# Performance work log

Hardware: AMD Instinct MI355X
Metric: run time of the kernel (lower is better)

The kernel has to match this reference:

```python
import jax, jax.numpy as jnp
import numpy as np

H, NH, HD, M, K = 768, 12, 64, 16, 4
BASE_LR, THETA = 1.0, 10000.0
EPS = 1e-5


def _freqs_cis():
    f = 1.0 / (THETA ** (np.arange(0, HD, 2)[: HD // 2].astype(np.float32) / HD))
    fr = np.outer(np.arange(2 * M), f).astype(np.float32)
    return jnp.asarray(np.complex64(np.cos(fr) + 1j * np.sin(fr)))  # [2M, HD//2]

FREQS = _freqs_cis()


def _rope(xq, xk, freqs):
    # xq, xk: [B,N,NH,HD]; freqs: [B,N,HD//2] complex64
    def rot(x):
        xr = x.astype(jnp.float32).reshape(*x.shape[:-1], -1, 2)
        xc = jax.lax.complex(xr[..., 0], xr[..., 1]) * freqs[:, :, None, :]
        return jnp.stack((jnp.real(xc), jnp.imag(xc)), -1).reshape(*x.shape)
    return rot(xq), rot(xk)


def _causal_conv(x, kern, bias):
    # x [B,N,C], kern [K,C]; module's left-pad + SAME conv => taps on x[t-K..t-1]
    B, N, C = x.shape
    y = jax.lax.conv_general_dilated(x, kern[:, None, :], (1,), [(K, 0)],
        dimension_numbers=('NWC', 'WIO', 'NWC'), feature_group_count=C)
    return y[:, :N] + bias


def _ln(x, g, b):
    mu = x.mean(-1, keepdims=True)
    v = x.var(-1, keepdims=True)
    return ((x - mu) / jnp.sqrt(v + EPS)) * g + b


def _ln_l2_bwd(x, tgt, g, b):
    # grad of 0.5*||LN(x) - tgt||^2 wrt x (fused, official TTT formulation)
    D = x.shape[-1]
    mu = x.mean(-1, keepdims=True)
    std = jnp.sqrt(x.var(-1, keepdims=True) + EPS)
    xh = (x - mu) / std
    gy = (g * xh + b - tgt) * g
    return (D * gy - gy.sum(-1, keepdims=True) - xh * (gy * xh).sum(-1, keepdims=True)) / (D * std)


def ttt_forward(hidden_states, position_ids, wq, wv, wo, wg,
                conv_q_kernel, conv_q_bias, conv_k_kernel, conv_k_bias,
                lr_w, lr_b, learnable_token_idx, ttt_gamma, ttt_beta,
                post_norm_scale, post_norm_bias, W1, b1):
    B, N, _ = hidden_states.shape
    nmb = N // M
    xqk = hidden_states @ wq  # shared pre-conv projection for Q and K
    XV = hidden_states @ wv
    XQ = _causal_conv(xqk, conv_q_kernel, conv_q_bias)
    XK = _causal_conv(xqk, conv_k_kernel, conv_k_bias)
    split = lambda x: x.reshape(B, N, NH, HD)
    XQ, XK, XV = split(XQ), split(XK), split(XV)
    freqs = FREQS[position_ids % M]  # [B,N,HD//2]
    XQ, XK = _rope(XQ, XK, freqs)
    # -> [nmb, B, NH, M, HD]
    mb = lambda x: x.reshape(B, nmb, M, NH, HD).transpose(1, 0, 3, 2, 4)
    XQ, XK, XV = mb(XQ), mb(XK), mb(XV)
    # eta [nmb,B,NH,M,M]: row i = token_idx lr schedule, col j = sigmoid lr of token j
    Xmb = hidden_states.reshape(B, nmb, M, H)
    lr = jax.nn.sigmoid(jnp.einsum('bnmw,hw->bhnm', Xmb, lr_w) + lr_b[None, :, None, None])
    tok = jnp.clip(learnable_token_idx + 1.0 / jnp.arange(1, M + 1, dtype=jnp.float32), 0.0)
    eta = (BASE_LR * tok)[None, None, None, :, None] * lr[:, :, :, None, :] / HD
    eta = eta.transpose(2, 0, 1, 3, 4)
    g = ttt_gamma[None]   # [1,NH,1,HD]
    bta = ttt_beta[None]
    tril = jnp.tril(jnp.ones((M, M), hidden_states.dtype))

    def step(carry, xs):
        W1c, b1c = carry  # [B,NH,HD,HD], [B,NH,1,HD]
        xq, xk, xv, et = xs
        Z1 = jnp.einsum('bhmd,bhde->bhme', xk, W1c) + b1c
        grad = _ln_l2_bwd(Z1, xv - xk, g, bta)  # [B,NH,M,HD]
        attn = tril * jnp.einsum('bhmd,bhnd->bhmn', xq, xk)
        b1_bar = b1c - jnp.einsum('bhmn,bhne->bhme', tril * et, grad)
        Z1_bar = jnp.einsum('bhmd,bhde->bhme', xq, W1c) - jnp.einsum('bhmn,bhne->bhme', et * attn, grad) + b1_bar
        last = et[..., -1, :, None]  # [B,NH,M,1] last row of eta
        W1n = W1c - jnp.einsum('bhmd,bhme->bhde', last * xk, grad)
        b1n = b1c - jnp.sum(last * grad, axis=-2, keepdims=True)
        return (W1n, b1n), xq + _ln(Z1_bar, g, bta)

    W1_0 = jnp.broadcast_to(W1[None], (B, NH, HD, HD))
    b1_0 = jnp.broadcast_to(b1[None], (B, NH, 1, HD))
    _, y = jax.lax.scan(step, (W1_0, b1_0), (XQ, XK, XV, eta))
    y = y.transpose(1, 0, 3, 2, 4).reshape(B, N, NH * HD)
    mu = y.mean(-1, keepdims=True)
    v = y.var(-1, keepdims=True)
    z = ((y - mu) / jnp.sqrt(v + EPS)) * post_norm_scale + post_norm_bias
    return (jax.nn.gelu(hidden_states @ wg) * z) @ wo


def setup_inputs() -> dict:
    key = jax.random.key(0)
    ks = jax.random.split(key, 10)
    B, N = 4, 2048
    s = 0.02
    return {
        'hidden_states': jax.random.normal(ks[0], (B, N, H), jnp.float32),
        'position_ids': jnp.arange(B * N, dtype=jnp.int32).reshape(B, N),
        'wq': jax.random.normal(ks[1], (H, NH * HD), jnp.float32) * s,
        'wv': jax.random.normal(ks[2], (H, NH * HD), jnp.float32) * s,
        'wo': jax.random.normal(ks[3], (NH * HD, H), jnp.float32) * s,
        'wg': jax.random.normal(ks[4], (H, H), jnp.float32) * s,
        'conv_q_kernel': jax.random.normal(ks[5], (K, H), jnp.float32) * s,
        'conv_q_bias': jnp.zeros((H,), jnp.float32),
        'conv_k_kernel': jax.random.normal(ks[6], (K, H), jnp.float32) * s,
        'conv_k_bias': jnp.zeros((H,), jnp.float32),
        'lr_w': jax.random.normal(ks[7], (NH, H), jnp.float32) * s,
        'lr_b': jnp.zeros((NH,), jnp.float32),
        'learnable_token_idx': jnp.zeros((M,), jnp.float32),
        'ttt_gamma': jnp.ones((NH, 1, HD), jnp.float32),
        'ttt_beta': jnp.zeros((NH, 1, HD), jnp.float32),
        'post_norm_scale': jnp.ones((NH * HD,), jnp.float32),
        'post_norm_bias': jnp.zeros((NH * HD,), jnp.float32),
        'W1': jax.random.normal(ks[8], (NH, HD, HD), jnp.float32) * s,
        'b1': jnp.zeros((NH, 1, HD), jnp.float32),
    }


def reference(hidden_states, position_ids, wq, wv, wo, wg,
              conv_q_kernel, conv_q_bias, conv_k_kernel, conv_k_bias,
              lr_w, lr_b, learnable_token_idx, ttt_gamma, ttt_beta,
              post_norm_scale, post_norm_bias, W1, b1):
    return ttt_forward(hidden_states, position_ids, wq, wv, wo, wg,
                       conv_q_kernel, conv_q_bias, conv_k_kernel, conv_k_bias,
                       lr_w, lr_b, learnable_token_idx, ttt_gamma, ttt_beta,
                       post_norm_scale, post_norm_bias, W1, b1)
```

## Files before the change

### kernel.cpp

```cpp
#include <hip/hip_runtime.h>
#include <math.h>

#define Hdim 768
#define NH 12
#define HD 64
#define MM 16
#define KK 4
#define Bb 4
#define Nn 2048
#define NMB 128
#define EPSV 1e-5f
#define PLD 2320
#define NCOLS 2316

__device__ float g_tab[1024];
__device__ float g_Wcat[(size_t)Hdim * PLD + 512];
__device__ float g_P[(size_t)Bb * Nn * PLD + 512];
__device__ float g_XQ[(size_t)Bb * NH * Nn * HD];
__device__ float g_XK[(size_t)Bb * NH * Nn * HD];
__device__ float g_XV[(size_t)Bb * NH * Nn * HD];
__device__ float g_lrv[(size_t)Bb * NH * Nn];
__device__ float g_y[(size_t)Bb * Nn * Hdim];

template <int CTRL>
__device__ __forceinline__ float dpp_mov(float x) {
    return __int_as_float(__builtin_amdgcn_update_dpp(
        0, __float_as_int(x), CTRL, 0xF, 0xF, true));
}
__device__ __forceinline__ float red16_dpp(float x) {
    x += dpp_mov<0xB1>(x);
    x += dpp_mov<0x4E>(x);
    x += dpp_mov<0x141>(x);
    x += dpp_mov<0x140>(x);
    return x;
}

__global__ __launch_bounds__(256) void prep_kernel(
    const float* __restrict__ wq, const float* __restrict__ wv,
    const float* __restrict__ wg, const float* __restrict__ lrw,
    float* __restrict__ Wcat, float* __restrict__ tab)
{
    int idx0 = blockIdx.x * 256 + threadIdx.x;
    if (idx0 < 512) {
        int pos = idx0 >> 5, k = idx0 & 31;
        double f = pow(10000.0, -(double)k / 32.0);
        double a = (double)pos * f;
        tab[2 * idx0 + 0] = (float)cos(a);
        tab[2 * idx0 + 1] = (float)sin(a);
    }
    const int total = Hdim * PLD;
    for (int i = idx0; i < total; i += 2048 * 256) {
        int k = i / PLD, j = i - k * PLD;
        float v;
        if (j < 768)       v = wq[k * 768 + j];
        else if (j < 1536) v = wv[k * 768 + (j - 768)];
        else if (j < 2304) v = wg[k * 768 + (j - 1536)];
        else if (j < NCOLS) v = lrw[(j - 2304) * 768 + k];
        else v = 0.f;
        Wcat[i] = v;
    }
}

__global__ __launch_bounds__(256) void gemm_tiled(
    const float* __restrict__ A, int lda,
    const float* __restrict__ Bm, int ldb,
    float* __restrict__ C, int ldc,
    int M, int N, int K)
{
    __shared__ float As[16][132];
    __shared__ float Bs[16][132];
    const int tid = threadIdx.x;
    const int tx = tid & 15, ty = tid >> 4;
    const int row0 = blockIdx.y * 128;
    const int col0 = blockIdx.x * 128;
    const int r_lo = ty * 4, c_lo = tx * 4;

    float acc[8][8];
#pragma unroll
    for (int i = 0; i < 8; ++i)
#pragma unroll
        for (int j = 0; j < 8; ++j) acc[i][j] = 0.f;

    for (int kt = 0; kt < K; kt += 16) {
#pragma unroll
        for (int i = 0; i < 2; ++i) {
            int id = tid + i * 256;
            int r = id >> 2, kq = (id & 3) * 4;
            const float4 a = *reinterpret_cast<const float4*>(
                &A[(size_t)(row0 + r) * lda + kt + kq]);
            As[kq + 0][r] = a.x; As[kq + 1][r] = a.y;
            As[kq + 2][r] = a.z; As[kq + 3][r] = a.w;
        }
#pragma unroll
        for (int i = 0; i < 2; ++i) {
            int id = tid + i * 256;
            int kr = id >> 5, jq = (id & 31) * 4;
            const float4 bv = *reinterpret_cast<const float4*>(
                &Bm[(size_t)(kt + kr) * ldb + col0 + jq]);
            *reinterpret_cast<float4*>(&Bs[kr][jq]) = bv;
        }
        __syncthreads();
#pragma unroll
        for (int k = 0; k < 16; ++k) {
            float a[8], bb[8];
            *reinterpret_cast<float4*>(&a[0]) = *reinterpret_cast<float4*>(&As[k][r_lo]);
            *reinterpret_cast<float4*>(&a[4]) = *reinterpret_cast<float4*>(&As[k][64 + r_lo]);
            *reinterpret_cast<float4*>(&bb[0]) = *reinterpret_cast<float4*>(&Bs[k][c_lo]);
            *reinterpret_cast<float4*>(&bb[4]) = *reinterpret_cast<float4*>(&Bs[k][64 + c_lo]);
#pragma unroll
            for (int i = 0; i < 8; ++i)
#pragma unroll
                for (int j = 0; j < 8; ++j)
                    acc[i][j] = fmaf(a[i], bb[j], acc[i][j]);
        }
        __syncthreads();
    }
#pragma unroll
    for (int i = 0; i < 8; ++i) {
        int rr = row0 + ((i < 4) ? (r_lo + i) : (64 + r_lo + i - 4));
        if (rr >= M) continue;
#pragma unroll
        for (int jb = 0; jb < 2; ++jb) {
            int cc = col0 + jb * 64 + c_lo;
            if (cc + 3 < N) {
                *reinterpret_cast<float4*>(&C[(size_t)rr * ldc + cc]) =
                    make_float4(acc[i][jb * 4 + 0], acc[i][jb * 4 + 1],
                                acc[i][jb * 4 + 2], acc[i][jb * 4 + 3]);
            } else {
#pragma unroll
                for (int jj = 0; jj < 4; ++jj)
                    if (cc + jj < N) C[(size_t)rr * ldc + cc + jj] = acc[i][jb * 4 + jj];
            }
        }
    }
}

__global__ __launch_bounds__(256) void conv_rope_kernel(
    const float* __restrict__ P, const int* __restrict__ pid,
    const float* __restrict__ cqk, const float* __restrict__ cqb,
    const float* __restrict__ ckk, const float* __restrict__ ckb,
    const float* __restrict__ lr_b, const float* __restrict__ tab,
    float* __restrict__ XQp, float* __restrict__ XKp, float* __restrict__ XVp,
    float* __restrict__ lrv)
{
    const int t = blockIdx.x;
    const int b = t >> 11, n = t & 2047;
    const int tid = threadIdx.x;
    __shared__ float xq_s[768], xk_s[768];
    const size_t rowP = (size_t)t * PLD;

#pragma unroll
    for (int i = 0; i < 3; ++i) {
        int c = tid + i * 256;
        float aq = cqb[c], ak = ckb[c];
#pragma unroll
        for (int w = 0; w < 4; ++w) {
            int np = n + w - 4;
            if (np >= 0) {
                float x = P[(size_t)(t + w - 4) * PLD + c];
                aq = fmaf(cqk[w * 768 + c], x, aq);
                ak = fmaf(ckk[w * 768 + c], x, ak);
            }
        }
        xq_s[c] = aq; xk_s[c] = ak;
        int h = c >> 6, d = c & 63;
        XVp[((size_t)(b * NH + h)) * (Nn * HD) + n * 64 + d] = P[rowP + 768 + c];
    }
    if (tid < NH) {
        float x = P[rowP + 2304 + tid] + lr_b[tid];
        lrv[((size_t)(b * NH + tid)) * Nn + n] = 1.f / (1.f + expf(-x));
    }
    __syncthreads();
    const int pos = pid[t] & 15;
    for (int p = tid; p < 384; p += 256) {
        int h = p >> 5, k = p & 31;
        float cv = tab[(pos * 32 + k) * 2 + 0];
        float sv = tab[(pos * 32 + k) * 2 + 1];
        int c0 = h * 64 + 2 * k;
        size_t base = ((size_t)(b * NH + h)) * (Nn * HD) + n * 64 + 2 * k;
        float x0 = xq_s[c0], x1 = xq_s[c0 + 1];
        XQp[base + 0] = x0 * cv - x1 * sv;
        XQp[base + 1] = x0 * sv + x1 * cv;
        x0 = xk_s[c0]; x1 = xk_s[c0 + 1];
        XKp[base + 0] = x0 * cv - x1 * sv;
        XKp[base + 1] = x0 * sv + x1 * cv;
    }
}

__global__ __launch_bounds__(256) void ttt_scan_kernel(
    const float* __restrict__ XQp, const float* __restrict__ XKp,
    const float* __restrict__ XVp, const float* __restrict__ lrv,
    const float* __restrict__ W1g, const float* __restrict__ b1g,
    const float* __restrict__ gam, const float* __restrict__ bet,
    const float* __restrict__ tokidx, float* __restrict__ ybuf)
{
    const int h = blockIdx.x, b = blockIdx.y;
    const int bh = b * NH + h;
    const int tid = threadIdx.x;
    const int e = tid & 63, q = tid >> 6;
    const int q16 = q * 16;

    __shared__ float xq_s[2][16][68], xk_s[2][16][68], xv_s[2][16][68];
    __shared__ float grad_s[16][68];
    __shared__ float part[2][4][16][64];
    __shared__ float b1_s[2][64], g_s[64], bt_s[64];
    __shared__ float lrs_s[2][16], tokv_s[16], alpha_s[16];
    __shared__ float coef_s[16][17];

    float W1own[16];
#pragma unroll
    for (int r = 0; r < 16; ++r)
        W1own[r] = W1g[h * 4096 + (q16 + r) * 64 + e];
    if (tid < 64) {
        b1_s[0][tid] = b1g[h * 64 + tid];
        g_s[tid]  = gam[h * 64 + tid];
        bt_s[tid] = bet[h * 64 + tid];
    }
    if (tid < 16)
        tokv_s[tid] = fmaxf(tokidx[tid] + 1.f / (float)(tid + 1), 0.f);

    const size_t base = (size_t)bh * (Nn * HD);
    const int m_st = tid >> 4, d_st = (tid & 15) * 4;

    float4 pfq, pfk, pfv;
    float pflr = 0.f;
    {
        size_t off = base + (size_t)tid * 4;
        pfq = *reinterpret_cast<const float4*>(XQp + off);
        pfk = *reinterpret_cast<const float4*>(XKp + off);
        pfv = *reinterpret_cast<const float4*>(XVp + off);
        if (tid < 16) pflr = lrv[(size_t)bh * Nn + tid];
    }
    *reinterpret_cast<float4*>(&xq_s[0][m_st][d_st]) = pfq;
    *reinterpret_cast<float4*>(&xk_s[0][m_st][d_st]) = pfk;
    *reinterpret_cast<float4*>(&xv_s[0][m_st][d_st]) = pfv;
    if (tid < 16) lrs_s[0][tid] = pflr;
    __syncthreads();

    float zb[4];
    int cur = 0;

    for (int c = 0; c < NMB; ++c) {
        const int nxt = cur ^ 1;

        {
            const int cn = (c < NMB - 1) ? (c + 1) : c;
            size_t off = base + (size_t)cn * 1024 + tid * 4;
            pfq = *reinterpret_cast<const float4*>(XQp + off);
            pfk = *reinterpret_cast<const float4*>(XKp + off);
            pfv = *reinterpret_cast<const float4*>(XVp + off);
            if (tid < 16) pflr = lrv[(size_t)bh * Nn + cn * 16 + tid];
        }
#pragma unroll
        for (int m = 0; m < 16; ++m) {
            float xkv[16], xqv[16];
            *reinterpret_cast<float4*>(&xkv[0])  = *reinterpret_cast<float4*>(&xk_s[cur][m][q16 + 0]);
            *reinterpret_cast<float4*>(&xkv[4])  = *reinterpret_cast<float4*>(&xk_s[cur][m][q16 + 4]);
            *reinterpret_cast<float4*>(&xkv[8])  = *reinterpret_cast<float4*>(&xk_s[cur][m][q16 + 8]);
            *reinterpret_cast<float4*>(&xkv[12]) = *reinterpret_cast<float4*>(&xk_s[cur][m][q16 + 12]);
            *reinterpret_cast<float4*>(&xqv[0])  = *reinterpret_cast<float4*>(&xq_s[cur][m][q16 + 0]);
            *reinterpret_cast<float4*>(&xqv[4])  = *reinterpret_cast<float4*>(&xq_s[cur][m][q16 + 4]);
            *reinterpret_cast<float4*>(&xqv[8])  = *reinterpret_cast<float4*>(&xq_s[cur][m][q16 + 8]);
            *reinterpret_cast<float4*>(&xqv[12]) = *reinterpret_cast<float4*>(&xq_s[cur][m][q16 + 12]);
            float az = 0.f, aq = 0.f;
#pragma unroll
            for (int r = 0; r < 16; ++r) {
                az = fmaf(xkv[r], W1own[r], az);
                aq = fmaf(xqv[r], W1own[r], aq);
            }
            part[0][q][m][e] = az;
            part[1][q][m][e] = aq;
        }
        __syncthreads();

        {
            *reinterpret_cast<float4*>(&xq_s[nxt][m_st][d_st]) = pfq;
            *reinterpret_cast<float4*>(&xk_s[nxt][m_st][d_st]) = pfk;
            *reinterpret_cast<float4*>(&xv_s[nxt][m_st][d_st]) = pfv;
            if (tid < 16) lrs_s[nxt][tid] = pflr;

            const int m = tid >> 4, e0 = (tid & 15) * 4;
            float4 p0 = *reinterpret_cast<float4*>(&part[0][0][m][e0]);
            float4 p1 = *reinterpret_cast<float4*>(&part[0][1][m][e0]);
            float4 p2 = *reinterpret_cast<float4*>(&part[0][2][m][e0]);
            float4 p3 = *reinterpret_cast<float4*>(&part[0][3][m][e0]);
            float4 q0 = *reinterpret_cast<float4*>(&part[1][0][m][e0]);
            float4 q1 = *reinterpret_cast<float4*>(&part[1][1][m][e0]);
            float4 q2 = *reinterpret_cast<float4*>(&part[1][2][m][e0]);
            float4 q3 = *reinterpret_cast<float4*>(&part[1][3][m][e0]);
            float z1[4];
            z1[0] = b1_s[cur][e0 + 0] + p0.x + p1.x + p2.x + p3.x;
            z1[1] = b1_s[cur][e0 + 1] + p0.y + p1.y + p2.y + p3.y;
            z1[2] = b1_s[cur][e0 + 2] + p0.z + p1.z + p2.z + p3.z;
            z1[3] = b1_s[cur][e0 + 3] + p0.w + p1.w + p2.w + p3.w;
            zb[0] = q0.x + q1.x + q2.x + q3.x;
            zb[1] = q0.y + q1.y + q2.y + q3.y;
            zb[2] = q0.z + q1.z + q2.z + q3.z;
            zb[3] = q0.w + q1.w + q2.w + q3.w;

            float lsum = red16_dpp(z1[0] + z1[1] + z1[2] + z1[3]);
            const float mu = lsum * (1.f / 64.f);
            float lss = 0.f;
#pragma unroll
            for (int jj = 0; jj < 4; ++jj) { float d = z1[jj] - mu; lss += d * d; }
            lss = red16_dpp(lss);
            const float rstd = 1.f / sqrtf(lss * (1.f / 64.f) + EPSV);
            float gy[4], xh[4], sgy = 0.f, sgx = 0.f;
#pragma unroll
            for (int jj = 0; jj < 4; ++jj) {
                int ee = e0 + jj;
                xh[jj] = (z1[jj] - mu) * rstd;
                float tgt = xv_s[cur][m][ee] - xk_s[cur][m][ee];
                gy[jj] = (g_s[ee] * xh[jj] + bt_s[ee] - tgt) * g_s[ee];
                sgy += gy[jj]; sgx += gy[jj] * xh[jj];
            }
            sgy = red16_dpp(sgy); sgx = red16_dpp(sgx);
            const float sc = rstd * (1.f / 64.f);
#pragma unroll
            for (int jj = 0; jj < 4; ++jj)
                grad_s[m][e0 + jj] = (64.f * gy[jj] - sgy - xh[jj] * sgx) * sc;

            const int i3 = m, j3 = (tid & 15);
            float cf = 0.f;
            if (j3 <= i3) {
                float s = 0.f;
#pragma unroll
                for (int d = 0; d < 64; d += 4) {
                    float4 a  = *reinterpret_cast<float4*>(&xq_s[cur][i3][d]);
                    float4 bq = *reinterpret_cast<float4*>(&xk_s[cur][j3][d]);
                    s += a.x * bq.x + a.y * bq.y + a.z * bq.z + a.w * bq.w;
                }
                cf = tokv_s[i3] * lrs_s[cur][j3] * (1.f / 64.f) * (1.f + s);
            }
            coef_s[i3][j3] = cf;
            if (tid < 16) alpha_s[tid] = tokv_s[15] * lrs_s[cur][tid] * (1.f / 64.f);
        }
        __syncthreads();

        {
            const int m = tid >> 4, e0 = (tid & 15) * 4;
            float zf[4];
#pragma unroll
            for (int jj = 0; jj < 4; ++jj) zf[jj] = zb[jj] + b1_s[cur][e0 + jj];
            for (int j = 0; j <= m; ++j) {
                float cfv = coef_s[m][j];
                float4 g4 = *reinterpret_cast<float4*>(&grad_s[j][e0]);
                zf[0] = fmaf(-cfv, g4.x, zf[0]);
                zf[1] = fmaf(-cfv, g4.y, zf[1]);
                zf[2] = fmaf(-cfv, g4.z, zf[2]);
                zf[3] = fmaf(-cfv, g4.w, zf[3]);
            }
            float lsum = red16_dpp(zf[0] + zf[1] + zf[2] + zf[3]);
            const float mu = lsum * (1.f / 64.f);
            float lss = 0.f;
#pragma unroll
            for (int jj = 0; jj < 4; ++jj) { float d = zf[jj] - mu; lss += d * d; }
            lss = red16_dpp(lss);
            const float rstd = 1.f / sqrtf(lss * (1.f / 64.f) + EPSV);
            float ov[4];
#pragma unroll
            for (int jj = 0; jj < 4; ++jj) {
                int ee = e0 + jj;
                ov[jj] = xq_s[cur][m][ee] + ((zf[jj] - mu) * rstd * g_s[ee] + bt_s[ee]);
            }
            size_t yoff = (size_t)(b * Nn + c * 16 + m) * 768 + h * 64 + e0;
            *reinterpret_cast<float4*>(&ybuf[yoff]) =
                make_float4(ov[0], ov[1], ov[2], ov[3]);
        }
        {
#pragma unroll
            for (int m = 0; m < 16; ++m) {
                float f = alpha_s[m] * grad_s[m][e];
                float xkv[16];
                *reinterpret_cast<float4*>(&xkv[0])  = *reinterpret_cast<float4*>(&xk_s[cur][m][q16 + 0]);
                *reinterpret_cast<float4*>(&xkv[4])  = *reinterpret_cast<float4*>(&xk_s[cur][m][q16 + 4]);
                *reinterpret_cast<float4*>(&xkv[8])  = *reinterpret_cast<float4*>(&xk_s[cur][m][q16 + 8]);
                *reinterpret_cast<float4*>(&xkv[12]) = *reinterpret_cast<float4*>(&xk_s[cur][m][q16 + 12]);
#pragma unroll
                for (int r = 0; r < 16; ++r)
                    W1own[r] = fmaf(-f, xkv[r], W1own[r]);
            }
            if (q == 0) {
                float sb = 0.f;
#pragma unroll
                for (int m = 0; m < 16; ++m)
                    sb += alpha_s[m] * grad_s[m][e];
                b1_s[nxt][e] = b1_s[cur][e] - sb;
            }
        }
        __syncthreads();
        cur = nxt;
    }
}

__global__ __launch_bounds__(256) void post_gate_kernel(
    const float* __restrict__ ybuf, const float* __restrict__ P,
    const float* __restrict__ ps, const float* __restrict__ pb,
    float* __restrict__ u)
{
    const int t = blockIdx.x;
    const int tid = threadIdx.x;
    __shared__ float red_a[4], red_b[4];
    float v[3];
    float lsum = 0.f;
#pragma unroll
    for (int i = 0; i < 3; ++i) {
        int c = tid + i * 256;
        v[i] = ybuf[(size_t)t * 768 + c];
        lsum += v[i];
    }
#pragma unroll
    for (int m = 1; m < 64; m <<= 1) lsum += __shfl_xor(lsum, m);
    if ((tid & 63) == 0) red_a[tid >> 6] = lsum;
    __syncthreads();
    const float mu = (red_a[0] + red_a[1] + red_a[2] + red_a[3]) * (1.f / 768.f);
    float lv = 0.f;
#pragma unroll
    for (int i = 0; i < 3; ++i) { float d = v[i] - mu; lv += d * d; }
#pragma unroll
    for (int m = 1; m < 64; m <<= 1) lv += __shfl_xor(lv, m);
    if ((tid & 63) == 0) red_b[tid >> 6] = lv;
    __syncthreads();
    const float var = (red_b[0] + red_b[1] + red_b[2] + red_b[3]) * (1.f / 768.f);
    const float rstd = 1.f / sqrtf(var + EPSV);
#pragma unroll
    for (int i = 0; i < 3; ++i) {
        int c = tid + i * 256;
        float g = P[(size_t)t * PLD + 1536 + c];
        float gl = 0.5f * g * (1.f + tanhf(0.7978845608028654f * (g + 0.044715f * g * g * g)));
        u[(size_t)t * 768 + c] = gl * ((v[i] - mu) * rstd * ps[c] + pb[c]);
    }
}

extern "C" void kernel_launch(void* const* d_in, const int* in_sizes, int n_in,
                              void* d_out, int out_size, void* d_ws, size_t ws_size,
                              hipStream_t stream)
{
    const float* hs   = (const float*)d_in[0];
    const int*   pid  = (const int*)  d_in[1];
    const float* wq   = (const float*)d_in[2];
    const float* wv   = (const float*)d_in[3];
    const float* wo   = (const float*)d_in[4];
    const float* wg   = (const float*)d_in[5];
    const float* cqk  = (const float*)d_in[6];
    const float* cqb  = (const float*)d_in[7];
    const float* ckk  = (const float*)d_in[8];
    const float* ckb  = (const float*)d_in[9];
    const float* lrw  = (const float*)d_in[10];
    const float* lrb  = (const float*)d_in[11];
    const float* lti  = (const float*)d_in[12];
    const float* gam  = (const float*)d_in[13];
    const float* bet  = (const float*)d_in[14];
    const float* ps   = (const float*)d_in[15];
    const float* pb   = (const float*)d_in[16];
    const float* W1g  = (const float*)d_in[17];
    const float* b1g  = (const float*)d_in[18];
    float* out = (float*)d_out;
    (void)d_ws; (void)ws_size; (void)in_sizes; (void)n_in; (void)out_size;

    float *tab = nullptr, *Wcat = nullptr, *P = nullptr, *XQp = nullptr,
          *XKp = nullptr, *XVp = nullptr, *lrv = nullptr, *ybuf = nullptr;
    hipGetSymbolAddress((void**)&tab,  HIP_SYMBOL(g_tab));
    hipGetSymbolAddress((void**)&Wcat, HIP_SYMBOL(g_Wcat));
    hipGetSymbolAddress((void**)&P,    HIP_SYMBOL(g_P));
    hipGetSymbolAddress((void**)&XQp,  HIP_SYMBOL(g_XQ));
    hipGetSymbolAddress((void**)&XKp,  HIP_SYMBOL(g_XK));
    hipGetSymbolAddress((void**)&XVp,  HIP_SYMBOL(g_XV));
    hipGetSymbolAddress((void**)&lrv,  HIP_SYMBOL(g_lrv));
    hipGetSymbolAddress((void**)&ybuf, HIP_SYMBOL(g_y));
    float* ubuf = XQp;

    hipLaunchKernelGGL(prep_kernel, dim3(2048), dim3(256), 0, stream,
                       wq, wv, wg, lrw, Wcat, tab);
    hipLaunchKernelGGL(gemm_tiled, dim3(19, 64), dim3(256), 0, stream,
                       hs, Hdim, Wcat, PLD, P, PLD, Bb * Nn, NCOLS, Hdim);
    hipLaunchKernelGGL(conv_rope_kernel, dim3(Bb * Nn), dim3(256), 0, stream,
                       P, pid, cqk, cqb, ckk, ckb, lrb, tab, XQp, XKp, XVp, lrv);
    hipLaunchKernelGGL(ttt_scan_kernel, dim3(NH, Bb), dim3(256), 0, stream,
                       XQp, XKp, XVp, lrv, W1g, b1g, gam, bet, lti, ybuf);
    hipLaunchKernelGGL(post_gate_kernel, dim3(Bb * Nn), dim3(256), 0, stream,
                       ybuf, P, ps, pb, ubuf);
    hipLaunchKernelGGL(gemm_tiled, dim3(6, 64), dim3(256), 0, stream,
                       ubuf, Hdim, wo, Hdim, out, Hdim, Bb * Nn, Hdim, Hdim);
}
```

Baseline: 1.262 ms.

## Read scan inputs straight from global memory instead of LDS double-buffering

Drops the shared-memory double buffers for XQ/XK/XV/lr in the TTT scan kernel and reads chunk rows directly from global memory. The row offset is forced wave-uniform with readfirstlane, so these reads can become scalar loads, and the part buffer is padded to 68 columns. This is meant to cut LDS traffic, shared-memory footprint and the store/prefetch staging, but it removes the explicit prefetch of the next chunk. It also reloads the same data several times per chunk from global or cache, which risks exposed memory latency on the serial scan.

```diff
diff --git a/kernel.cpp b/kernel.cpp
--- a/kernel.cpp
+++ b/kernel.cpp
@@ -199,12 +199,12 @@
     const int tid = threadIdx.x;
     const int e = tid & 63, q = tid >> 6;
     const int q16 = q * 16;
-
-    __shared__ float xq_s[2][16][68], xk_s[2][16][68], xv_s[2][16][68];
+    const int q16u = __builtin_amdgcn_readfirstlane(q16);
+
+    __shared__ float part[2][4][16][68];
     __shared__ float grad_s[16][68];
-    __shared__ float part[2][4][16][64];
     __shared__ float b1_s[2][64], g_s[64], bt_s[64];
-    __shared__ float lrs_s[2][16], tokv_s[16], alpha_s[16];
+    __shared__ float tokv_s[16], alpha_s[16];
     __shared__ float coef_s[16][17];
 
     float W1own[16];
@@ -220,65 +220,61 @@
         tokv_s[tid] = fmaxf(tokidx[tid] + 1.f / (float)(tid + 1), 0.f);
 
     const size_t base = (size_t)bh * (Nn * HD);
-    const int m_st = tid >> 4, d_st = (tid & 15) * 4;
-
-    float4 pfq, pfk, pfv;
-    float pflr = 0.f;
-    {
-        size_t off = base + (size_t)tid * 4;
-        pfq = *reinterpret_cast<const float4*>(XQp + off);
-        pfk = *reinterpret_cast<const float4*>(XKp + off);
-        pfv = *reinterpret_cast<const float4*>(XVp + off);
-        if (tid < 16) pflr = lrv[(size_t)bh * Nn + tid];
-    }
-    *reinterpret_cast<float4*>(&xq_s[0][m_st][d_st]) = pfq;
-    *reinterpret_cast<float4*>(&xk_s[0][m_st][d_st]) = pfk;
-    *reinterpret_cast<float4*>(&xv_s[0][m_st][d_st]) = pfv;
-    if (tid < 16) lrs_s[0][tid] = pflr;
+    const float* __restrict__ lrC0 = lrv + (size_t)bh * Nn;
     __syncthreads();
 
     float zb[4];
-    int cur = 0;
 
     for (int c = 0; c < NMB; ++c) {
-        const int nxt = cur ^ 1;
+        const int cur = c & 1, nxt = cur ^ 1;
+        const float* __restrict__ xkC = XKp + base + (size_t)c * 1024;
+        const float* __restrict__ xqC = XQp + base + (size_t)c * 1024;
+        const float* __restrict__ xvC = XVp + base + (size_t)c * 1024;
+        const float* __restrict__ lrC = lrC0 + c * 16;
+
+#pragma unroll
+        for (int mb = 0; mb < 4; ++mb) {
+            float xrow[4][16];
+#pragma unroll
+            for (int mm = 0; mm < 4; ++mm) {
+                const float* rp = xkC + (mb * 4 + mm) * 64 + q16u;
+                *reinterpret_cast<float4*>(&xrow[mm][0])  = *reinterpret_cast<const float4*>(rp + 0);
+                *reinterpret_cast<float4*>(&xrow[mm][4])  = *reinterpret_cast<const float4*>(rp + 4);
+                *reinterpret_cast<float4*>(&xrow[mm][8])  = *reinterpret_cast<const float4*>(rp + 8);
+                *reinterpret_cast<float4*>(&xrow[mm][12]) = *reinterpret_cast<const float4*>(rp + 12);
+            }
+#pragma unroll
+            for (int mm = 0; mm < 4; ++mm) {
+                float az = 0.f;
+#pragma unroll
+                for (int r = 0; r < 16; ++r)
+                    az = fmaf(xrow[mm][r], W1own[r], az);
+                part[0][q][mb * 4 + mm][e] = az;
+            }
+        }
+#pragma unroll
+        for (int mb = 0; mb < 4; ++mb) {
+            float xrow[4][16];
+#pragma unroll
+            for (int mm = 0; mm < 4; ++mm) {
+                const float* rp = xqC + (mb * 4 + mm) * 64 + q16u;
+                *reinterpret_cast<float4*>(&xrow[mm][0])  = *reinterpret_cast<const float4*>(rp + 0);
+                *reinterpret_cast<float4*>(&xrow[mm][4])  = *reinterpret_cast<const float4*>(rp + 4);
+                *reinterpret_cast<float4*>(&xrow[mm][8])  = *reinterpret_cast<const float4*>(rp + 8);
+                *reinterpret_cast<float4*>(&xrow[mm][12]) = *reinterpret_cast<const float4*>(rp + 12);
+            }
+#pragma unroll
+            for (int mm = 0; mm < 4; ++mm) {
+                float aq = 0.f;
+#pragma unroll
+                for (int r = 0; r < 16; ++r)
+                    aq = fmaf(xrow[mm][r], W1own[r], aq);
+                part[1][q][mb * 4 + mm][e] = aq;
+            }
+        }
+        __syncthreads();
 
         {
-            const int cn = (c < NMB - 1) ? (c + 1) : c;
-            size_t off = base + (size_t)cn * 1024 + tid * 4;
-            pfq = *reinterpret_cast<const float4*>(XQp + off);
-            pfk = *reinterpret_cast<const float4*>(XKp + off);
-            pfv = *reinterpret_cast<const float4*>(XVp + off);
-            if (tid < 16) pflr = lrv[(size_t)bh * Nn + cn * 16 + tid];
-        }
-#pragma unroll
-        for (int m = 0; m < 16; ++m) {
-            float xkv[16], xqv[16];
-            *reinterpret_cast<float4*>(&xkv[0])  = *reinterpret_cast<float4*>(&xk_s[cur][m][q16 + 0]);
-            *reinterpret_cast<float4*>(&xkv[4])  = *reinterpret_cast<float4*>(&xk_s[cur][m][q16 + 4]);
-            *reinterpret_cast<float4*>(&xkv[8])  = *reinterpret_cast<float4*>(&xk_s[cur][m][q16 + 8]);
-            *reinterpret_cast<float4*>(&xkv[12]) = *reinterpret_cast<float4*>(&xk_s[cur][m][q16 + 12]);
-            *reinterpret_cast<float4*>(&xqv[0])  = *reinterpret_cast<float4*>(&xq_s[cur][m][q16 + 0]);
-            *reinterpret_cast<float4*>(&xqv[4])  = *reinterpret_cast<float4*>(&xq_s[cur][m][q16 + 4]);
-            *reinterpret_cast<float4*>(&xqv[8])  = *reinterpret_cast<float4*>(&xq_s[cur][m][q16 + 8]);
-            *reinterpret_cast<float4*>(&xqv[12]) = *reinterpret_cast<float4*>(&xq_s[cur][m][q16 + 12]);
-            float az = 0.f, aq = 0.f;
-#pragma unroll
-            for (int r = 0; r < 16; ++r) {
-                az = fmaf(xkv[r], W1own[r], az);
-                aq = fmaf(xqv[r], W1own[r], aq);
-            }
-            part[0][q][m][e] = az;
-            part[1][q][m][e] = aq;
-        }
-        __syncthreads();
-
-        {
-            *reinterpret_cast<float4*>(&xq_s[nxt][m_st][d_st]) = pfq;
-            *reinterpret_cast<float4*>(&xk_s[nxt][m_st][d_st]) = pfk;
-            *reinterpret_cast<float4*>(&xv_s[nxt][m_st][d_st]) = pfv;
-            if (tid < 16) lrs_s[nxt][tid] = pflr;
-
             const int m = tid >> 4, e0 = (tid & 15) * 4;
             float4 p0 = *reinterpret_cast<float4*>(&part[0][0][m][e0]);
             float4 p1 = *reinterpret_cast<float4*>(&part[0][1][m][e0]);
@@ -305,13 +301,17 @@
             for (int jj = 0; jj < 4; ++jj) { float d = z1[jj] - mu; lss += d * d; }
             lss = red16_dpp(lss);
             const float rstd = 1.f / sqrtf(lss * (1.f / 64.f) + EPSV);
+
+            const float4 xvv = *reinterpret_cast<const float4*>(xvC + m * 64 + e0);
+            const float4 xkk = *reinterpret_cast<const float4*>(xkC + m * 64 + e0);
+            const float tgt4[4] = { xvv.x - xkk.x, xvv.y - xkk.y,
+                                    xvv.z - xkk.z, xvv.w - xkk.w };
             float gy[4], xh[4], sgy = 0.f, sgx = 0.f;
 #pragma unroll
             for (int jj = 0; jj < 4; ++jj) {
                 int ee = e0 + jj;
                 xh[jj] = (z1[jj] - mu) * rstd;
-                float tgt = xv_s[cur][m][ee] - xk_s[cur][m][ee];
-                gy[jj] = (g_s[ee] * xh[jj] + bt_s[ee] - tgt) * g_s[ee];
+                gy[jj] = (g_s[ee] * xh[jj] + bt_s[ee] - tgt4[jj]) * g_s[ee];
                 sgy += gy[jj]; sgx += gy[jj] * xh[jj];
             }
             sgy = red16_dpp(sgy); sgx = red16_dpp(sgx);
@@ -325,15 +325,15 @@
             if (j3 <= i3) {
                 float s = 0.f;
 #pragma unroll
-                for (int d = 0; d < 64; d += 4) {
-                    float4 a  = *reinterpret_cast<float4*>(&xq_s[cur][i3][d]);
-                    float4 bq = *reinterpret_cast<float4*>(&xk_s[cur][j3][d]);
+                for (int dq = 0; dq < 16; ++dq) {
+                    float4 a  = *reinterpret_cast<const float4*>(xqC + i3 * 64 + dq * 4);
+                    float4 bq = *reinterpret_cast<const float4*>(xkC + j3 * 64 + dq * 4);
                     s += a.x * bq.x + a.y * bq.y + a.z * bq.z + a.w * bq.w;
                 }
-                cf = tokv_s[i3] * lrs_s[cur][j3] * (1.f / 64.f) * (1.f + s);
+                cf = tokv_s[i3] * lrC[j3] * (1.f / 64.f) * (1.f + s);
             }
             coef_s[i3][j3] = cf;
-            if (tid < 16) alpha_s[tid] = tokv_s[15] * lrs_s[cur][tid] * (1.f / 64.f);
+            if (tid < 16) alpha_s[tid] = tokv_s[15] * lrC[tid] * (1.f / 64.f);
         }
         __syncthreads();
 
@@ -357,11 +357,13 @@
             for (int jj = 0; jj < 4; ++jj) { float d = zf[jj] - mu; lss += d * d; }
             lss = red16_dpp(lss);
             const float rstd = 1.f / sqrtf(lss * (1.f / 64.f) + EPSV);
+            const float4 xqv = *reinterpret_cast<const float4*>(xqC + m * 64 + e0);
+            const float xq4[4] = { xqv.x, xqv.y, xqv.z, xqv.w };
             float ov[4];
 #pragma unroll
             for (int jj = 0; jj < 4; ++jj) {
                 int ee = e0 + jj;
-                ov[jj] = xq_s[cur][m][ee] + ((zf[jj] - mu) * rstd * g_s[ee] + bt_s[ee]);
+                ov[jj] = xq4[jj] + ((zf[jj] - mu) * rstd * g_s[ee] + bt_s[ee]);
             }
             size_t yoff = (size_t)(b * Nn + c * 16 + m) * 768 + h * 64 + e0;
             *reinterpret_cast<float4*>(&ybuf[yoff]) =
@@ -369,16 +371,24 @@
         }
         {
 #pragma unroll
-            for (int m = 0; m < 16; ++m) {
-                float f = alpha_s[m] * grad_s[m][e];
-                float xkv[16];
-                *reinterpret_cast<float4*>(&xkv[0])  = *reinterpret_cast<float4*>(&xk_s[cur][m][q16 + 0]);
-                *reinterpret_cast<float4*>(&xkv[4])  = *reinterpret_cast<float4*>(&xk_s[cur][m][q16 + 4]);
-                *reinterpret_cast<float4*>(&xkv[8])  = *reinterpret_cast<float4*>(&xk_s[cur][m][q16 + 8]);
-                *reinterpret_cast<float4*>(&xkv[12]) = *reinterpret_cast<float4*>(&xk_s[cur][m][q16 + 12]);
-#pragma unroll
-                for (int r = 0; r < 16; ++r)
-                    W1own[r] = fmaf(-f, xkv[r], W1own[r]);
+            for (int mb = 0; mb < 4; ++mb) {
+                float xrow[4][16];
+#pragma unroll
+                for (int mm = 0; mm < 4; ++mm) {
+                    const float* rp = xkC + (mb * 4 + mm) * 64 + q16u;
+                    *reinterpret_cast<float4*>(&xrow[mm][0])  = *reinterpret_cast<const float4*>(rp + 0);
+                    *reinterpret_cast<float4*>(&xrow[mm][4])  = *reinterpret_cast<const float4*>(rp + 4);
+                    *reinterpret_cast<float4*>(&xrow[mm][8])  = *reinterpret_cast<const float4*>(rp + 8);
+                    *reinterpret_cast<float4*>(&xrow[mm][12]) = *reinterpret_cast<const float4*>(rp + 12);
+                }
+#pragma unroll
+                for (int mm = 0; mm < 4; ++mm) {
+                    const int m = mb * 4 + mm;
+                    float f = alpha_s[m] * grad_s[m][e];
+#pragma unroll
+                    for (int r = 0; r < 16; ++r)
+                        W1own[r] = fmaf(-f, xrow[mm][r], W1own[r]);
+                }
             }
             if (q == 0) {
                 float sb = 0.f;
@@ -389,7 +399,6 @@
             }
         }
         __syncthreads();
-        cur = nxt;
     }
 }
 
```

Result: slower. 1.764 ms (+39.8%).

## Run projection GEMMs on MFMA using split-bf16x3 emulation of fp32

Applied to the files above, without the earlier changes.

Both fp32 GEMMs are replaced by a kernel that splits each operand into high and low bf16 halves in shared memory and accumulates three bf16 MFMA products per tile, approximating fp32 accuracy on the matrix cores. A one-wave probe kernel checks at runtime that the MFMA fragment layout gives correct results, and the GEMM falls back to the old SIMT path if it does not. This aims to cut the FMA-bound cost of the two large projections. The price is conversion overhead, strided scalar loads of B, scalar output stores, a small accuracy loss against true fp32, and one extra kernel launch.

```diff
diff --git a/kernel.cpp b/kernel.cpp
--- a/kernel.cpp
+++ b/kernel.cpp
@@ -13,6 +13,9 @@
 #define PLD 2320
 #define NCOLS 2316
 
+typedef __attribute__((ext_vector_type(8))) short short8;
+typedef __attribute__((ext_vector_type(4))) float f32x4;
+
 __device__ float g_tab[1024];
 __device__ float g_Wcat[(size_t)Hdim * PLD + 512];
 __device__ float g_P[(size_t)Bb * Nn * PLD + 512];
@@ -21,6 +24,7 @@
 __device__ float g_XV[(size_t)Bb * NH * Nn * HD];
 __device__ float g_lrv[(size_t)Bb * NH * Nn];
 __device__ float g_y[(size_t)Bb * Nn * Hdim];
+__device__ int   g_mfma_ok;
 
 template <int CTRL>
 __device__ __forceinline__ float dpp_mov(float x) {
@@ -33,6 +37,44 @@
     x += dpp_mov<0x141>(x);
     x += dpp_mov<0x140>(x);
     return x;
+}
+
+__device__ __forceinline__ void cvt2(float a, float b, unsigned &hi, unsigned &lo) {
+    unsigned ua = __float_as_uint(a); unsigned ra = (ua + 0x7FFFu + ((ua >> 16) & 1u)) >> 16;
+    unsigned ub = __float_as_uint(b); unsigned rb = (ub + 0x7FFFu + ((ub >> 16) & 1u)) >> 16;
+    hi = ra | (rb << 16);
+    float la = a - __uint_as_float(ra << 16);
+    float lb = b - __uint_as_float(rb << 16);
+    unsigned ula = __float_as_uint(la); ula = (ula + 0x7FFFu + ((ula >> 16) & 1u)) >> 16;
+    unsigned ulb = __float_as_uint(lb); ulb = (ulb + 0x7FFFu + ((ulb >> 16) & 1u)) >> 16;
+    lo = ula | (ulb << 16);
+}
+
+__global__ void mfma_probe() {
+    const int l = threadIdx.x;
+    short8 af, bf;
+#pragma unroll
+    for (int j = 0; j < 8; ++j) {
+        int k = (l >> 4) * 8 + j;
+        int r = l & 15;
+        float aval = (float)(((r * 5 + k * 3) % 7) - 3);
+        float bval = (float)(((k * 11 + (l & 15) * 2) % 5) - 2);
+        af[j] = (short)(__float_as_uint(aval) >> 16);
+        bf[j] = (short)(__float_as_uint(bval) >> 16);
+    }
+    f32x4 z = {0.f, 0.f, 0.f, 0.f};
+    f32x4 d = __builtin_amdgcn_mfma_f32_16x16x32_bf16(af, bf, z, 0, 0, 0);
+    bool ok = true;
+#pragma unroll
+    for (int i = 0; i < 4; ++i) {
+        int row = (l >> 4) * 4 + i, col = l & 15;
+        int ref = 0;
+        for (int k = 0; k < 32; ++k)
+            ref += (((row * 5 + k * 3) % 7) - 3) * (((k * 11 + col * 2) % 5) - 2);
+        ok = ok && (fabsf(d[i] - (float)ref) < 0.5f);
+    }
+    unsigned long long m = __ballot(ok);
+    if (l == 0) g_mfma_ok = (m == 0xFFFFFFFFFFFFFFFFULL) ? 1 : 0;
 }
 
 __global__ __launch_bounds__(256) void prep_kernel(
@@ -61,18 +103,107 @@
     }
 }
 
-__global__ __launch_bounds__(256) void gemm_tiled(
+__global__ __launch_bounds__(256) void gemm_bf16x3(
     const float* __restrict__ A, int lda,
     const float* __restrict__ Bm, int ldb,
     float* __restrict__ C, int ldc,
     int M, int N, int K)
 {
-    __shared__ float As[16][132];
-    __shared__ float Bs[16][132];
+    __shared__ unsigned smem[10240];
     const int tid = threadIdx.x;
-    const int tx = tid & 15, ty = tid >> 4;
     const int row0 = blockIdx.y * 128;
     const int col0 = blockIdx.x * 128;
+
+    if (g_mfma_ok) {
+        unsigned* Ah = smem;
+        unsigned* Al = smem + 2560;
+        unsigned* Bh = smem + 5120;
+        unsigned* Bl = smem + 7680;
+        const int lane = tid & 63, wv = tid >> 6;
+        const int wr = wv >> 1, wc = wv & 1;
+        const int l15 = lane & 15, lg = lane >> 4;
+
+        f32x4 acc[4][4];
+#pragma unroll
+        for (int i = 0; i < 4; ++i)
+#pragma unroll
+            for (int j = 0; j < 4; ++j) acc[i][j] = f32x4{0.f, 0.f, 0.f, 0.f};
+
+        const int bcol = tid & 127, bkh = tid >> 7;
+
+        for (int kt = 0; kt < K; kt += 32) {
+            if (kt) __syncthreads();
+#pragma unroll
+            for (int it = 0; it < 4; ++it) {
+                int id = tid + it * 256;
+                int r = id >> 3, kq = (id & 7) * 4;
+                const float4 av = *reinterpret_cast<const float4*>(
+                    &A[(size_t)(row0 + r) * lda + kt + kq]);
+                unsigned h0, l0, h1, l1;
+                cvt2(av.x, av.y, h0, l0);
+                cvt2(av.z, av.w, h1, l1);
+                int idx = r * 20 + (kq >> 1);
+                Ah[idx] = h0; Ah[idx + 1] = h1;
+                Al[idx] = l0; Al[idx + 1] = l1;
+            }
+            {
+                float bv[16];
+#pragma unroll
+                for (int j = 0; j < 16; ++j)
+                    bv[j] = Bm[(size_t)(kt + bkh * 16 + j) * ldb + col0 + bcol];
+                unsigned hb[8], lb[8];
+#pragma unroll
+                for (int t = 0; t < 8; ++t)
+                    cvt2(bv[2 * t], bv[2 * t + 1], hb[t], lb[t]);
+                int base = bcol * 20 + bkh * 8;
+                *reinterpret_cast<uint4*>(&Bh[base])     = *reinterpret_cast<uint4*>(&hb[0]);
+                *reinterpret_cast<uint4*>(&Bh[base + 4]) = *reinterpret_cast<uint4*>(&hb[4]);
+                *reinterpret_cast<uint4*>(&Bl[base])     = *reinterpret_cast<uint4*>(&lb[0]);
+                *reinterpret_cast<uint4*>(&Bl[base + 4]) = *reinterpret_cast<uint4*>(&lb[4]);
+            }
+            __syncthreads();
+            short8 ahf[4], alf[4], bhf[4], blf[4];
+#pragma unroll
+            for (int fr = 0; fr < 4; ++fr) {
+                int idx = (wr * 64 + fr * 16 + l15) * 20 + lg * 4;
+                ahf[fr] = *reinterpret_cast<short8*>(&Ah[idx]);
+                alf[fr] = *reinterpret_cast<short8*>(&Al[idx]);
+            }
+#pragma unroll
+            for (int fc = 0; fc < 4; ++fc) {
+                int idx = (wc * 64 + fc * 16 + l15) * 20 + lg * 4;
+                bhf[fc] = *reinterpret_cast<short8*>(&Bh[idx]);
+                blf[fc] = *reinterpret_cast<short8*>(&Bl[idx]);
+            }
+#pragma unroll
+            for (int fr = 0; fr < 4; ++fr)
+#pragma unroll
+                for (int fc = 0; fc < 4; ++fc) {
+                    acc[fr][fc] = __builtin_amdgcn_mfma_f32_16x16x32_bf16(
+                        ahf[fr], bhf[fc], acc[fr][fc], 0, 0, 0);
+                    acc[fr][fc] = __builtin_amdgcn_mfma_f32_16x16x32_bf16(
+                        ahf[fr], blf[fc], acc[fr][fc], 0, 0, 0);
+                    acc[fr][fc] = __builtin_amdgcn_mfma_f32_16x16x32_bf16(
+                        alf[fr], bhf[fc], acc[fr][fc], 0, 0, 0);
+                }
+        }
+#pragma unroll
+        for (int fr = 0; fr < 4; ++fr)
+#pragma unroll
+            for (int fc = 0; fc < 4; ++fc) {
+                int col = col0 + wc * 64 + fc * 16 + l15;
+                if (col >= N) continue;
+                int rbase = row0 + wr * 64 + fr * 16 + lg * 4;
+#pragma unroll
+                for (int i = 0; i < 4; ++i)
+                    C[(size_t)(rbase + i) * ldc + col] = acc[fr][fc][i];
+            }
+        return;
+    }
+
+    float* As = reinterpret_cast<float*>(smem);
+    float* Bs = As + 16 * 132;
+    const int tx = tid & 15, ty = tid >> 4;
     const int r_lo = ty * 4, c_lo = tx * 4;
 
     float acc[8][8];
@@ -88,8 +219,8 @@
             int r = id >> 2, kq = (id & 3) * 4;
             const float4 a = *reinterpret_cast<const float4*>(
                 &A[(size_t)(row0 + r) * lda + kt + kq]);
-            As[kq + 0][r] = a.x; As[kq + 1][r] = a.y;
-            As[kq + 2][r] = a.z; As[kq + 3][r] = a.w;
+            As[(kq + 0) * 132 + r] = a.x; As[(kq + 1) * 132 + r] = a.y;
+            As[(kq + 2) * 132 + r] = a.z; As[(kq + 3) * 132 + r] = a.w;
         }
 #pragma unroll
         for (int i = 0; i < 2; ++i) {
@@ -97,16 +228,16 @@
             int kr = id >> 5, jq = (id & 31) * 4;
             const float4 bv = *reinterpret_cast<const float4*>(
                 &Bm[(size_t)(kt + kr) * ldb + col0 + jq]);
-            *reinterpret_cast<float4*>(&Bs[kr][jq]) = bv;
+            *reinterpret_cast<float4*>(&Bs[kr * 132 + jq]) = bv;
         }
         __syncthreads();
 #pragma unroll
         for (int k = 0; k < 16; ++k) {
             float a[8], bb[8];
-            *reinterpret_cast<float4*>(&a[0]) = *reinterpret_cast<float4*>(&As[k][r_lo]);
-            *reinterpret_cast<float4*>(&a[4]) = *reinterpret_cast<float4*>(&As[k][64 + r_lo]);
-            *reinterpret_cast<float4*>(&bb[0]) = *reinterpret_cast<float4*>(&Bs[k][c_lo]);
-            *reinterpret_cast<float4*>(&bb[4]) = *reinterpret_cast<float4*>(&Bs[k][64 + c_lo]);
+            *reinterpret_cast<float4*>(&a[0]) = *reinterpret_cast<float4*>(&As[k * 132 + r_lo]);
+            *reinterpret_cast<float4*>(&a[4]) = *reinterpret_cast<float4*>(&As[k * 132 + 64 + r_lo]);
+            *reinterpret_cast<float4*>(&bb[0]) = *reinterpret_cast<float4*>(&Bs[k * 132 + c_lo]);
+            *reinterpret_cast<float4*>(&bb[4]) = *reinterpret_cast<float4*>(&Bs[k * 132 + 64 + c_lo]);
 #pragma unroll
             for (int i = 0; i < 8; ++i)
 #pragma unroll
@@ -470,9 +601,10 @@
     hipGetSymbolAddress((void**)&ybuf, HIP_SYMBOL(g_y));
     float* ubuf = XQp;
 
+    hipLaunchKernelGGL(mfma_probe, dim3(1), dim3(64), 0, stream);
     hipLaunchKernelGGL(prep_kernel, dim3(2048), dim3(256), 0, stream,
                        wq, wv, wg, lrw, Wcat, tab);
-    hipLaunchKernelGGL(gemm_tiled, dim3(19, 64), dim3(256), 0, stream,
+    hipLaunchKernelGGL(gemm_bf16x3, dim3(19, 64), dim3(256), 0, stream,
                        hs, Hdim, Wcat, PLD, P, PLD, Bb * Nn, NCOLS, Hdim);
     hipLaunchKernelGGL(conv_rope_kernel, dim3(Bb * Nn), dim3(256), 0, stream,
                        P, pid, cqk, cqb, ckk, ckb, lrb, tab, XQp, XKp, XVp, lrv);
@@ -480,6 +612,6 @@
                        XQp, XKp, XVp, lrv, W1g, b1g, gam, bet, lti, ybuf);
     hipLaunchKernelGGL(post_gate_kernel, dim3(Bb * Nn), dim3(256), 0, stream,
                        ybuf, P, ps, pb, ubuf);
-    hipLaunchKernelGGL(gemm_tiled, dim3(6, 64), dim3(256), 0, stream,
+    hipLaunchKernelGGL(gemm_bf16x3, dim3(6, 64), dim3(256), 0, stream,
                        ubuf, Hdim, wo, Hdim, out, Hdim, Bb * Nn, Hdim, Hdim);
 }
```

New measurement: 1.098 ms. 13.0% less time.
